# Optimization experiments

Hardware: AMD Instinct MI355X
Metric: run time of the kernel (lower is better)

## Reference

```python
import jax, jax.numpy as jnp
import numpy as np

D_MODEL = 512
N_HEADS = 8
D_HEAD = D_MODEL // N_HEADS  # 64
D_PROJ = 32
H_ENC = 512
D_MAX = 32


def _rope_cache(T, d):
    pos = jnp.arange(T, dtype=jnp.float32)[:, None]                      # [T,1]
    freqs = 1.0 / (10000.0 ** (jnp.arange(0, d, 2, dtype=jnp.float32) / d))  # [d/2]
    ang = pos * freqs                                                     # [T,d/2]
    return jnp.cos(ang), jnp.sin(ang)


def _apply_rope(x, cos, sin):
    # x: [B,H,T,D]
    T = x.shape[2]
    d2 = x.shape[-1] // 2
    x1, x2 = x[..., :d2], x[..., d2:]
    c = cos[:T][None, None]
    s = sin[:T][None, None]
    return jnp.concatenate([x1 * c - x2 * s, x2 * c + x1 * s], axis=-1)


def _layernorm(a, g, b, eps=1e-5):
    m = jnp.mean(a, axis=-1, keepdims=True)
    v = jnp.mean((a - m) ** 2, axis=-1, keepdims=True)
    return (a - m) * jax.lax.rsqrt(v + eps) * g + b


def setup_inputs() -> dict:
    key = jax.random.key(0)
    ks = jax.random.split(key, 8)
    B, T = 2, 2048
    x = jax.random.normal(ks[0], (B, T, D_MODEL), jnp.float32)
    q_projs = jax.random.normal(ks[1], (N_HEADS, D_MODEL, D_PROJ), jnp.float32) * D_MODEL ** -0.5
    k_projs = jax.random.normal(ks[2], (N_HEADS, D_MODEL, D_PROJ), jnp.float32) * D_MODEL ** -0.5
    w_v = jax.random.normal(ks[3], (D_MODEL, D_MODEL), jnp.float32) * D_MODEL ** -0.5
    w_proj = jax.random.normal(ks[4], (D_MODEL, D_MODEL), jnp.float32) * 0.02
    q_gain = jnp.ones((N_HEADS,), jnp.float32)
    enc_w0 = jax.random.normal(ks[5], (H_ENC, D_MODEL), jnp.float32) * D_MODEL ** -0.5
    enc_ln1_g = jnp.ones((H_ENC,), jnp.float32)
    enc_ln1_b = jnp.zeros((H_ENC,), jnp.float32)
    enc_w1 = jax.random.normal(ks[6], (H_ENC, H_ENC), jnp.float32) * H_ENC ** -0.5
    enc_ln2_g = jnp.ones((H_ENC,), jnp.float32)
    enc_ln2_b = jnp.zeros((H_ENC,), jnp.float32)
    enc_w2 = jax.random.normal(ks[7], (H_ENC, H_ENC), jnp.float32) * H_ENC ** -0.5
    enc_w_out = jax.random.normal(jax.random.fold_in(key, 99), (D_MAX, H_ENC), jnp.float32) * H_ENC ** -0.5
    coord_temp = jnp.ones((D_MAX,), jnp.float32)
    return {"x": x, "q_projs": q_projs, "k_projs": k_projs, "w_v": w_v, "w_proj": w_proj,
            "q_gain": q_gain, "enc_w0": enc_w0, "enc_ln1_g": enc_ln1_g, "enc_ln1_b": enc_ln1_b,
            "enc_w1": enc_w1, "enc_ln2_g": enc_ln2_g, "enc_ln2_b": enc_ln2_b, "enc_w2": enc_w2,
            "enc_w_out": enc_w_out, "coord_temp": coord_temp}


def reference(x, q_projs, k_projs, w_v, w_proj, q_gain,
              enc_w0, enc_ln1_g, enc_ln1_b, enc_w1, enc_ln2_g, enc_ln2_b,
              enc_w2, enc_w_out, coord_temp):
    B, T, C = x.shape
    # ---- CausalSelfAttention (qk_mode='per_head_proj') ----
    q = jnp.einsum('btd,hdo->bhto', x, q_projs)                    # [B,H,T,Dp]
    k = jnp.einsum('btd,hdo->bhto', x, k_projs)                    # [B,H,T,Dp]
    v = (x @ w_v.T).reshape(B, T, N_HEADS, D_HEAD).transpose(0, 2, 1, 3)  # [B,H,T,Dh]
    cos, sin = _rope_cache(T, D_PROJ)
    q = _apply_rope(q, cos, sin)
    k = _apply_rope(k, cos, sin)
    q = q * q_gain[None, :, None, None]
    scale = 1.0 / jnp.sqrt(jnp.asarray(D_PROJ, q.dtype))
    scores = jnp.einsum('bhto,bhso->bhts', q, k) * scale           # [B,H,T,T]
    causal = jnp.tril(jnp.ones((T, T), bool))
    scores = jnp.where(causal, scores, jnp.asarray(-1e30, scores.dtype))
    attn = jax.nn.softmax(scores, axis=-1)
    y = jnp.einsum('bhts,bhsd->bhtd', attn, v)                     # [B,H,T,Dh]
    # self-alignment subtraction (F.normalize eps = 1e-12)
    v_norm = v / jnp.maximum(jnp.linalg.norm(v, axis=-1, keepdims=True), 1e-12)
    self_align = jnp.sum(y * v_norm, axis=-1, keepdims=True) * v_norm
    y = y - self_align
    y = y.transpose(0, 2, 1, 3).reshape(B, T, C)
    h = x + y @ w_proj.T                                           # residual
    # ---- ChartEncoder (d_in == H so proj0 is Identity) ----
    he = h @ enc_w0.T
    he = h + jax.nn.silu(_layernorm(he, enc_ln1_g, enc_ln1_b) @ enc_w1.T)
    he = he + jax.nn.silu(_layernorm(he, enc_ln2_g, enc_ln2_b) @ enc_w2.T)
    h_rms = he * jax.lax.rsqrt(jnp.mean(he * he, axis=-1, keepdims=True) + 1e-6)
    z_raw = h_rms @ enc_w_out.T                                    # [B,T,d_max]
    z = jnp.tanh(z_raw / (jax.nn.softplus(coord_temp) + 1e-4))
    return z
```

## Files before the change

### kernel.cpp

```cpp
#include <hip/hip_runtime.h>
#include <math.h>

typedef unsigned short u16;
typedef __attribute__((ext_vector_type(8))) short short8;
typedef __attribute__((ext_vector_type(4))) float floatx4;

__device__ __forceinline__ float b2f(u16 u) { return __uint_as_float(((unsigned)u) << 16); }
__device__ __forceinline__ u16 f2b(float f) {
  unsigned u = __float_as_uint(f);
  return (u16)((u + 0x7fffu + ((u >> 16) & 1u)) >> 16);
}

__global__ __launch_bounds__(256) void prep_cast(const float* __restrict__ x, const float* __restrict__ wpr,
                                                 const float* __restrict__ w0, const float* __restrict__ w1,
                                                 const float* __restrict__ w2, const float* __restrict__ qp,
                                                 const float* __restrict__ kp, const float* __restrict__ wv,
                                                 u16* __restrict__ XB, u16* __restrict__ WPRb,
                                                 u16* __restrict__ W0b, u16* __restrict__ W1b,
                                                 u16* __restrict__ W2b, u16* __restrict__ wcat) {
  int bi = blockIdx.x, tid = threadIdx.x;
  if (bi < 2048) {
    int i = bi * 256 + tid;
    float4 v = ((const float4*)x)[i];
    ushort4 o; o.x = f2b(v.x); o.y = f2b(v.y); o.z = f2b(v.z); o.w = f2b(v.w);
    ((ushort4*)XB)[i] = o;
  } else if (bi < 3072) {
    int i = (bi - 2048) * 256 + tid;
    int sel = i >> 16, j = i & 65535;
    const float* s = sel == 0 ? wpr : sel == 1 ? w0 : sel == 2 ? w1 : w2;
    float4 v = ((const float4*)s)[j];
    ushort4 o; o.x = f2b(v.x); o.y = f2b(v.y); o.z = f2b(v.z); o.w = f2b(v.w);
    if (sel == 0) {
      ((ushort4*)WPRb)[j] = o;
    } else {
      u16* d = sel == 1 ? W0b : sel == 2 ? W1b : W2b;
      int n = j >> 7, k4 = (j & 127) << 2;
      int lane = (((k4 >> 3) & 3) << 4) | (n & 15);
      int dst = (((n >> 4) * 16 + (k4 >> 5)) << 9) + lane * 8 + (k4 & 7);
      *(ushort4*)(d + dst) = o;
    }
  } else {
    int i = (bi - 3072) * 256 + tid;
    int d = i & 511, c = i >> 9;
    float v;
    if (c < 512) {
      int hh = c >> 5, o = c & 31;
      const float* src = (hh < 8) ? qp : kp;
      int h = hh & 7;
      v = src[(h * 512 + d) * 32 + o];
    } else {
      v = wv[(c - 512) * 512 + d];
    }
    wcat[i] = f2b(v);
  }
}

template <int EPI, bool DUAL>
__global__ __launch_bounds__(256) void mgemm(const u16* __restrict__ A, const u16* __restrict__ Bw,
                                             const float* __restrict__ X, float* __restrict__ C,
                                             u16* __restrict__ Cb, int N) {
  __shared__ u16 As[64][72];
  __shared__ u16 Bs[64][72];
  const int tid = threadIdx.x;
  const int bm = blockIdx.y, bn = blockIdx.x;
  const int lane = tid & 63, wave = tid >> 6;
  const int wm = wave >> 1, wn = wave & 1;
  const int quad = lane >> 4, l16 = lane & 15;
  const int sr = tid >> 2;
  const int sk = (tid & 3) << 4;
  floatx4 acc[2][2] = {};
  const u16* Ap = A + (size_t)(bm * 64 + sr) * 512 + sk;
  const u16* Bp = Bw + (size_t)(bn * 64 + sr) * 512 + sk;
  uint4 a0 = *(const uint4*)(Ap);
  uint4 a1 = *(const uint4*)(Ap + 8);
  uint4 b0 = *(const uint4*)(Bp);
  uint4 b1 = *(const uint4*)(Bp + 8);
  for (int k0 = 0; k0 < 512; k0 += 64) {
    __syncthreads();
    *(uint4*)&As[sr][sk] = a0;
    *(uint4*)&As[sr][sk + 8] = a1;
    *(uint4*)&Bs[sr][sk] = b0;
    *(uint4*)&Bs[sr][sk + 8] = b1;
    __syncthreads();
    if (k0 + 64 < 512) {
      a0 = *(const uint4*)(Ap + k0 + 64);
      a1 = *(const uint4*)(Ap + k0 + 72);
      b0 = *(const uint4*)(Bp + k0 + 64);
      b1 = *(const uint4*)(Bp + k0 + 72);
    }
#pragma unroll
    for (int kk = 0; kk < 2; kk++) {
      short8 af0 = *(const short8*)&As[wm * 32 + l16][kk * 32 + quad * 8];
      short8 af1 = *(const short8*)&As[wm * 32 + 16 + l16][kk * 32 + quad * 8];
      short8 bf0 = *(const short8*)&Bs[wn * 32 + l16][kk * 32 + quad * 8];
      short8 bf1 = *(const short8*)&Bs[wn * 32 + 16 + l16][kk * 32 + quad * 8];
      acc[0][0] = __builtin_amdgcn_mfma_f32_16x16x32_bf16(af0, bf0, acc[0][0], 0, 0, 0);
      acc[0][1] = __builtin_amdgcn_mfma_f32_16x16x32_bf16(af0, bf1, acc[0][1], 0, 0, 0);
      acc[1][0] = __builtin_amdgcn_mfma_f32_16x16x32_bf16(af1, bf0, acc[1][0], 0, 0, 0);
      acc[1][1] = __builtin_amdgcn_mfma_f32_16x16x32_bf16(af1, bf1, acc[1][1], 0, 0, 0);
    }
  }
#pragma unroll
  for (int mt = 0; mt < 2; mt++)
#pragma unroll
    for (int r = 0; r < 4; r++) {
      int row = bm * 64 + wm * 32 + mt * 16 + quad * 4 + r;
#pragma unroll
      for (int nt = 0; nt < 2; nt++) {
        int col = bn * 64 + wn * 32 + nt * 16 + l16;
        float v = acc[mt][nt][r];
        if (EPI == 1) {
          v += X[(size_t)row * 512 + col];
        } else if (EPI == 2) {
          float xv = X[(size_t)row * 512 + col];
          v = xv + v / (1.f + __expf(-v));
        }
        C[(size_t)row * N + col] = v;
        if (DUAL) Cb[(size_t)row * N + col] = f2b(v);
      }
    }
}

__global__ __launch_bounds__(256) void prep_attn(const float* __restrict__ qkv, const float* __restrict__ qgain,
                                                 u16* __restrict__ qr, u16* __restrict__ kr,
                                                 u16* __restrict__ Vt) {
  const int bi = blockIdx.x, tid = threadIdx.x;
  if (bi < 2048) {
    int gid = bi * 256 + tid;
    int o = gid & 15;
    int t = (gid >> 4) & 2047;
    int h = (gid >> 15) & 7;
    int b = gid >> 18;
    const float* row = qkv + (size_t)(b * 2048 + t) * 1024;
    float freq = powf(10000.f, -(float)o / 16.f);
    float ang = (float)t * freq;
    float s, c;
    sincosf(ang, &s, &c);
    float g = qgain[h] * (0.17677669529663687f * 1.4426950408889634f);
    int qb = h * 32;
    float q0 = row[qb + o], q1 = row[qb + o + 16];
    float k0 = row[256 + qb + o], k1 = row[256 + qb + o + 16];
    u16* qo = qr + ((size_t)((b * 8 + h) * 2048 + t)) * 32;
    u16* ko = kr + ((size_t)((b * 8 + h) * 2048 + t)) * 32;
    qo[o] = f2b((q0 * c - q1 * s) * g);
    qo[o + 16] = f2b((q1 * c + q0 * s) * g);
    ko[o] = f2b(k0 * c - k1 * s);
    ko[o + 16] = f2b(k1 * c + k0 * s);
  } else {
    int idx = bi - 2048;
    const int tt = idx & 31, bh = idx >> 5;
    const int b = bh >> 3, h = bh & 7;
    __shared__ u16 Ts[64][72];
    const int r = tid >> 2, q = tid & 3;
    const float* src = qkv + ((size_t)(b * 2048 + tt * 64 + r)) * 1024 + 512 + h * 64 + q * 16;
#pragma unroll
    for (int j = 0; j < 4; j++) {
      float4 v = *(const float4*)(src + j * 4);
      Ts[q * 16 + j * 4 + 0][r] = f2b(v.x);
      Ts[q * 16 + j * 4 + 1][r] = f2b(v.y);
      Ts[q * 16 + j * 4 + 2][r] = f2b(v.z);
      Ts[q * 16 + j * 4 + 3][r] = f2b(v.w);
    }
    __syncthreads();
    u16* dst = Vt + ((size_t)(bh * 64 + r)) * 2048 + tt * 64 + q * 16;
    *(uint4*)dst = *(const uint4*)&Ts[r][q * 16];
    *(uint4*)(dst + 8) = *(const uint4*)&Ts[r][q * 16 + 8];
  }
}

__global__ __launch_bounds__(256) void attn_split(const u16* __restrict__ Qb, const u16* __restrict__ Kb,
                                                  const u16* __restrict__ Vt, float* __restrict__ PO,
                                                  float* __restrict__ PL) {
  const int bi = blockIdx.x;
  const int bh = bi & 15;
  const int q0i = (bi >> 4) & 15;
  const int rem = bi >> 8;
  const int qt = (rem & 1) ? (31 - q0i) : q0i;
  const int s = rem >> 1;
  const int tid = threadIdx.x;
  const int w = tid >> 6, lane = tid & 63, quad = lane >> 4, l16 = lane & 15;
  __shared__ u16 Vts[64][72];
  __shared__ u16 Ps[4][16][72];

  const int mid = (qt + 1) >> 1;
  const int kt_beg = s ? mid : 0;
  const int kt_end = s ? (qt + 1) : mid;

  short8 qfrag = *(const short8*)(Qb + ((size_t)(bh * 2048 + qt * 64 + w * 16 + l16)) * 32 + quad * 8);
  floatx4 o_acc[4] = {};
  float l_part[4] = {0.f, 0.f, 0.f, 0.f};
  const u16* Kbase = Kb + (size_t)bh * 2048 * 32;
  const u16* Vtb = Vt + (size_t)bh * 64 * 2048;
  const int vr = tid >> 2, vc = (tid & 3) << 4;

  uint4 v0 = {}, v1 = {};
  short8 kf[4] = {};
  if (kt_beg < kt_end) {
    const u16* src = Vtb + (size_t)vr * 2048 + kt_beg * 64 + vc;
    v0 = *(const uint4*)src;
    v1 = *(const uint4*)(src + 8);
#pragma unroll
    for (int nt = 0; nt < 4; nt++)
      kf[nt] = *(const short8*)(Kbase + (size_t)(kt_beg * 64 + nt * 16 + l16) * 32 + quad * 8);
  }

  for (int kt = kt_beg; kt < kt_end; ++kt) {
    __syncthreads();
    *(uint4*)&Vts[vr][vc] = v0;
    *(uint4*)&Vts[vr][vc + 8] = v1;
    __syncthreads();
    const bool more = (kt + 1 < kt_end);
    uint4 v0n = {}, v1n = {};
    short8 kfn[4] = {};
    if (more) {
      const u16* src = Vtb + (size_t)vr * 2048 + (kt + 1) * 64 + vc;
      v0n = *(const uint4*)src;
      v1n = *(const uint4*)(src + 8);
#pragma unroll
      for (int nt = 0; nt < 4; nt++)
        kfn[nt] = *(const short8*)(Kbase + (size_t)((kt + 1) * 64 + nt * 16 + l16) * 32 + quad * 8);
    }

    floatx4 s_acc[4];
#pragma unroll
    for (int nt = 0; nt < 4; nt++) {
      floatx4 zz = {0.f, 0.f, 0.f, 0.f};
      s_acc[nt] = __builtin_amdgcn_mfma_f32_16x16x32_bf16(qfrag, kf[nt], zz, 0, 0, 0);
    }
    const bool diag = (kt == qt);
#pragma unroll
    for (int r = 0; r < 4; r++) {
      int mloc = w * 16 + quad * 4 + r;
      float psum = 0.f;
#pragma unroll
      for (int nt = 0; nt < 4; nt++) {
        float p = __builtin_amdgcn_exp2f(s_acc[nt][r]);
        if (diag && (nt * 16 + l16) > mloc) p = 0.f;
        psum += p;
        Ps[w][quad * 4 + r][nt * 16 + l16] = f2b(p);
      }
      l_part[r] += psum;
    }
#pragma unroll
    for (int kc = 0; kc < 2; kc++) {
      short8 pf = *(const short8*)&Ps[w][l16][kc * 32 + quad * 8];
#pragma unroll
      for (int nt = 0; nt < 4; nt++) {
        short8 vf = *(const short8*)&Vts[nt * 16 + l16][kc * 32 + quad * 8];
        o_acc[nt] = __builtin_amdgcn_mfma_f32_16x16x32_bf16(pf, vf, o_acc[nt], 0, 0, 0);
      }
    }
    v0 = v0n; v1 = v1n;
#pragma unroll
    for (int nt = 0; nt < 4; nt++) kf[nt] = kfn[nt];
  }

  const int pidx = (bh * 32 + qt) * 2 + s;
  float* pob = PO + (size_t)pidx * 4096;
#pragma unroll
  for (int r = 0; r < 4; r++) {
    float ls = l_part[r];
#pragma unroll
    for (int mk = 1; mk < 16; mk <<= 1) ls += __shfl_xor(ls, mk, 64);
    int row = w * 16 + quad * 4 + r;
#pragma unroll
    for (int nt = 0; nt < 4; nt++) pob[row * 64 + nt * 16 + l16] = o_acc[nt][r];
    if (l16 == 0) PL[pidx * 64 + row] = ls;
  }
}

__global__ __launch_bounds__(256) void attn_combine(const float* __restrict__ PO, const float* __restrict__ PL,
                                                    const float* __restrict__ qkv, u16* __restrict__ y2b) {
  int ridx = blockIdx.x * 4 + (threadIdx.x >> 6);
  int lane = threadIdx.x & 63;
  int bh = ridx >> 11, tok = ridx & 2047;
  int qt = tok >> 6, row = tok & 63;
  int pidx = (bh * 32 + qt) * 2;
  const float* p0 = PO + (size_t)pidx * 4096 + row * 64;
  float o = p0[lane] + p0[4096 + lane];
  float l = PL[pidx * 64 + row] + PL[(pidx + 1) * 64 + row];
  float yv = o / l;
  int b = bh >> 3, h = bh & 7;
  float vv = qkv[(size_t)(b * 2048 + tok) * 1024 + 512 + h * 64 + lane];
  float ss = vv * vv, dot = yv * vv;
#pragma unroll
  for (int mk = 1; mk < 64; mk <<= 1) {
    ss += __shfl_xor(ss, mk, 64);
    dot += __shfl_xor(dot, mk, 64);
  }
  float coef = dot / fmaxf(ss, 1e-24f);
  y2b[(size_t)(b * 2048 + tok) * 512 + h * 64 + lane] = f2b(yv - coef * vv);
}

#define HPAD 516

__device__ __forceinline__ int enc_swz(int row, int col) {
  return row * 512 + ((((col >> 3) ^ (row & 7)) << 3) | (col & 7));
}

__device__ __forceinline__ void enc_gemm(const u16* __restrict__ inb, const u16* __restrict__ Wf,
                                         floatx4* acc, int wave, int l16, int quad, int lane) {
  const u16* wb = Wf + ((size_t)(wave * 4 * 16) << 9) + lane * 8;
  short8 aB[4];
  short8 bB[4][4];
#pragma unroll
  for (int p = 0; p < 4; p++) {
    aB[p] = *(const short8*)(inb + enc_swz(l16, p * 32 + quad * 8));
#pragma unroll
    for (int nt = 0; nt < 4; nt++)
      bB[p][nt] = *(const short8*)(wb + (((nt * 16) + p) << 9));
  }
#pragma unroll
  for (int ks = 0; ks < 16; ks++) {
    const int cur = ks & 3;
#pragma unroll
    for (int nt = 0; nt < 4; nt++)
      acc[nt] = __builtin_amdgcn_mfma_f32_16x16x32_bf16(aB[cur], bB[cur][nt], acc[nt], 0, 0, 0);
    if (ks + 4 < 16) {
      aB[cur] = *(const short8*)(inb + enc_swz(l16, (ks + 4) * 32 + quad * 8));
#pragma unroll
      for (int nt = 0; nt < 4; nt++)
        bB[cur][nt] = *(const short8*)(wb + (((nt * 16) + (ks + 4)) << 9));
    }
  }
}

__global__ __launch_bounds__(512) void enc_fused(const float* __restrict__ H, const u16* __restrict__ W0b,
                                                 const u16* __restrict__ W1b, const u16* __restrict__ W2b,
                                                 const float* __restrict__ g1v, const float* __restrict__ b1v,
                                                 const float* __restrict__ g2v, const float* __restrict__ b2v,
                                                 const float* __restrict__ wout, const float* __restrict__ ct,
                                                 float* __restrict__ z) {
  __shared__ u16 curb[16 * 512];
  __shared__ u16 lnb[16 * 512];
  __shared__ float hres[16][HPAD];
  __shared__ float red[8][16][2];

  const int tid = threadIdx.x;
  const int wave = tid >> 6, lane = tid & 63, quad = lane >> 4, l16 = lane & 15;
  const int row0 = blockIdx.x * 16;
  const int n0 = wave * 64;

#pragma unroll
  for (int j = 0; j < 4; j++) {
    int idx = j * 512 + tid;
    int row = idx >> 7, c4 = idx & 127;
    float4 v = ((const float4*)H)[(size_t)(row0 + row) * 128 + c4];
    *(float4*)&hres[row][c4 * 4] = v;
    int col = c4 * 4;
    curb[enc_swz(row, col + 0)] = f2b(v.x);
    curb[enc_swz(row, col + 1)] = f2b(v.y);
    curb[enc_swz(row, col + 2)] = f2b(v.z);
    curb[enc_swz(row, col + 3)] = f2b(v.w);
  }
  __syncthreads();

  floatx4 acc1[4] = {};
  enc_gemm(curb, W0b, acc1, wave, l16, quad, lane);

  {
#pragma unroll
    for (int r = 0; r < 4; r++) {
      float s = 0.f, q = 0.f;
#pragma unroll
      for (int nt = 0; nt < 4; nt++) { float v = acc1[nt][r]; s += v; q = fmaf(v, v, q); }
#pragma unroll
      for (int mk = 1; mk < 16; mk <<= 1) { s += __shfl_xor(s, mk, 64); q += __shfl_xor(q, mk, 64); }
      if (l16 == 0) { red[wave][quad * 4 + r][0] = s; red[wave][quad * 4 + r][1] = q; }
    }
    __syncthreads();
#pragma unroll
    for (int r = 0; r < 4; r++) {
      int R = quad * 4 + r;
      float st = 0.f, qt2 = 0.f;
#pragma unroll
      for (int w2 = 0; w2 < 8; w2++) { st += red[w2][R][0]; qt2 += red[w2][R][1]; }
      float mean = st * (1.f / 512.f);
      float inv = rsqrtf(qt2 * (1.f / 512.f) - mean * mean + 1e-5f);
#pragma unroll
      for (int nt = 0; nt < 4; nt++) {
        int col = n0 + nt * 16 + l16;
        lnb[enc_swz(R, col)] = f2b((acc1[nt][r] - mean) * inv * g1v[col] + b1v[col]);
      }
    }
    __syncthreads();
  }

  floatx4 acc2[4] = {};
  enc_gemm(lnb, W1b, acc2, wave, l16, quad, lane);
  float hval[4][4];
  {
#pragma unroll
    for (int r = 0; r < 4; r++) {
      int R = quad * 4 + r;
      float s = 0.f, q = 0.f;
#pragma unroll
      for (int nt = 0; nt < 4; nt++) {
        int col = n0 + nt * 16 + l16;
        float u = acc2[nt][r];
        float hv = hres[R][col] + u / (1.f + __expf(-u));
        hres[R][col] = hv;
        hval[nt][r] = hv;
        s += hv; q = fmaf(hv, hv, q);
      }
#pragma unroll
      for (int mk = 1; mk < 16; mk <<= 1) { s += __shfl_xor(s, mk, 64); q += __shfl_xor(q, mk, 64); }
      if (l16 == 0) { red[wave][R][0] = s; red[wave][R][1] = q; }
    }
    __syncthreads();
#pragma unroll
    for (int r = 0; r < 4; r++) {
      int R = quad * 4 + r;
      float st = 0.f, qt2 = 0.f;
#pragma unroll
      for (int w2 = 0; w2 < 8; w2++) { st += red[w2][R][0]; qt2 += red[w2][R][1]; }
      float mean = st * (1.f / 512.f);
      float inv = rsqrtf(qt2 * (1.f / 512.f) - mean * mean + 1e-5f);
#pragma unroll
      for (int nt = 0; nt < 4; nt++) {
        int col = n0 + nt * 16 + l16;
        lnb[enc_swz(R, col)] = f2b((hval[nt][r] - mean) * inv * g2v[col] + b2v[col]);
      }
    }
    __syncthreads();
  }

  floatx4 acc3[4] = {};
  enc_gemm(lnb, W2b, acc3, wave, l16, quad, lane);
  {
#pragma unroll
    for (int r = 0; r < 4; r++) {
      int R = quad * 4 + r;
      float q = 0.f;
#pragma unroll
      for (int nt = 0; nt < 4; nt++) {
        int col = n0 + nt * 16 + l16;
        float u = acc3[nt][r];
        float hv = hres[R][col] + u / (1.f + __expf(-u));
        hres[R][col] = hv;
        q = fmaf(hv, hv, q);
      }
#pragma unroll
      for (int mk = 1; mk < 16; mk <<= 1) q += __shfl_xor(q, mk, 64);
      if (l16 == 0) red[wave][R][1] = q;
    }
    __syncthreads();
  }

  {
    const int n = lane & 31, kh = lane >> 5;
    float rinv[2], pacc[2] = {0.f, 0.f};
#pragma unroll
    for (int rr = 0; rr < 2; rr++) {
      int R = wave * 2 + rr;
      float qt2 = 0.f;
#pragma unroll
      for (int w2 = 0; w2 < 8; w2++) qt2 += red[w2][R][1];
      rinv[rr] = rsqrtf(qt2 * (1.f / 512.f) + 1e-6f);
    }
    for (int kc = 0; kc < 64; kc++) {
      int k = kh * 256 + kc * 4;
      float4 wv = *(const float4*)(wout + (size_t)n * 512 + k);
#pragma unroll
      for (int rr = 0; rr < 2; rr++) {
        float4 hv = *(const float4*)&hres[wave * 2 + rr][k];
        pacc[rr] = fmaf(wv.x, hv.x, fmaf(wv.y, hv.y, fmaf(wv.z, hv.z, fmaf(wv.w, hv.w, pacc[rr]))));
      }
    }
#pragma unroll
    for (int rr = 0; rr < 2; rr++) pacc[rr] += __shfl_xor(pacc[rr], 32, 64);
    if (kh == 0) {
      float c = ct[n];
      float sp = (c > 20.f) ? c : log1pf(__expf(c));
#pragma unroll
      for (int rr = 0; rr < 2; rr++)
        z[(size_t)(row0 + wave * 2 + rr) * 32 + n] = tanhf(pacc[rr] * rinv[rr] / (sp + 1e-4f));
    }
  }
}

extern "C" void kernel_launch(void* const* d_in, const int* in_sizes, int n_in,
                              void* d_out, int out_size, void* d_ws, size_t ws_size,
                              hipStream_t stream) {
  const float* x = (const float*)d_in[0];
  const float* qp = (const float*)d_in[1];
  const float* kp = (const float*)d_in[2];
  const float* wv = (const float*)d_in[3];
  const float* wpr = (const float*)d_in[4];
  const float* qg = (const float*)d_in[5];
  const float* w0 = (const float*)d_in[6];
  const float* g1 = (const float*)d_in[7];
  const float* b1 = (const float*)d_in[8];
  const float* w1 = (const float*)d_in[9];
  const float* g2 = (const float*)d_in[10];
  const float* b2 = (const float*)d_in[11];
  const float* w2 = (const float*)d_in[12];
  const float* wout = (const float*)d_in[13];
  const float* ct = (const float*)d_in[14];
  float* z = (float*)d_out;

  float* ws = (float*)d_ws;
  const size_t MEG = 1024 * 1024;
  float* A_QKV = ws;
  u16* A_Qb = (u16*)(ws + 4 * MEG);
  u16* A_Kb = (u16*)(ws + 4 * MEG + 524288);
  u16* A_Vt = (u16*)(ws + 5 * MEG);
  float* A_PO = ws + 6 * MEG;
  u16* A_Y2b = (u16*)(ws + 10 * MEG);
  float* A_H = ws + 11 * MEG;
  u16* XB = (u16*)(ws + 13 * MEG);
  float* A_PL = ws + 13 * MEG;
  u16* WCATb = (u16*)(ws + 14 * MEG);
  u16* WPRb = WCATb + 524288;
  u16* W0b = WPRb + 262144;
  u16* W1b = W0b + 262144;
  u16* W2b = W1b + 262144;

  hipLaunchKernelGGL(prep_cast, dim3(5120), dim3(256), 0, stream, x, wpr, w0, w1, w2, qp, kp, wv,
                     XB, WPRb, W0b, W1b, W2b, WCATb);
  hipLaunchKernelGGL((mgemm<0, false>), dim3(16, 64), dim3(256), 0, stream, XB, WCATb,
                     (const float*)nullptr, A_QKV, (u16*)nullptr, 1024);
  hipLaunchKernelGGL(prep_attn, dim3(2560), dim3(256), 0, stream, A_QKV, qg, A_Qb, A_Kb, A_Vt);
  hipLaunchKernelGGL(attn_split, dim3(1024), dim3(256), 0, stream, A_Qb, A_Kb, A_Vt, A_PO, A_PL);
  hipLaunchKernelGGL(attn_combine, dim3(8192), dim3(256), 0, stream, A_PO, A_PL, A_QKV, A_Y2b);
  hipLaunchKernelGGL((mgemm<1, false>), dim3(8, 64), dim3(256), 0, stream, A_Y2b, WPRb, x, A_H,
                     (u16*)nullptr, 512);
  hipLaunchKernelGGL(enc_fused, dim3(256), dim3(512), 0, stream, A_H, W0b, W1b, W2b,
                     g1, b1, g2, b2, wout, ct, z);
}
```

Measured before the change: 191.7 us.

## Stream encoder weights through LDS with double-buffered direct global-to-LDS loads

Replaces per-wave register prefetch of the weight fragments (a 4-deep software pipeline in registers) with asynchronous global_load_lds copies into a double-buffered LDS staging area, one k-chunk ahead. The aim is to cut register pressure and overlap weight fetch with MFMA work. In exchange it adds 64 KB of shared memory per block, which lowers occupancy, and a block-wide barrier on every k step. Prefetch depth also drops from four chunks to one.

```diff
diff --git a/kernel.cpp b/kernel.cpp
--- a/kernel.cpp
+++ b/kernel.cpp
@@ -299,29 +299,34 @@
 }
 
 __device__ __forceinline__ void enc_gemm(const u16* __restrict__ inb, const u16* __restrict__ Wf,
-                                         floatx4* acc, int wave, int l16, int quad, int lane) {
-  const u16* wb = Wf + ((size_t)(wave * 4 * 16) << 9) + lane * 8;
-  short8 aB[4];
-  short8 bB[4][4];
-#pragma unroll
-  for (int p = 0; p < 4; p++) {
-    aB[p] = *(const short8*)(inb + enc_swz(l16, p * 32 + quad * 8));
-#pragma unroll
-    for (int nt = 0; nt < 4; nt++)
-      bB[p][nt] = *(const short8*)(wb + (((nt * 16) + p) << 9));
-  }
-#pragma unroll
-  for (int ks = 0; ks < 16; ks++) {
-    const int cur = ks & 3;
-#pragma unroll
-    for (int nt = 0; nt < 4; nt++)
-      acc[nt] = __builtin_amdgcn_mfma_f32_16x16x32_bf16(aB[cur], bB[cur][nt], acc[nt], 0, 0, 0);
-    if (ks + 4 < 16) {
-      aB[cur] = *(const short8*)(inb + enc_swz(l16, (ks + 4) * 32 + quad * 8));
+                                         u16* __restrict__ Wst, floatx4* acc,
+                                         int wave, int lane, int l16, int quad) {
+  const int wslot = (wave * 4) * 512;
+  const int src_lane = lane * 8;
+#pragma unroll
+  for (int nt = 0; nt < 4; nt++)
+    __builtin_amdgcn_global_load_lds(
+        (const __attribute__((address_space(1))) void*)(Wf + ((size_t)((wave * 4 + nt) * 16) << 9) + src_lane),
+        (__attribute__((address_space(3))) void*)(Wst + wslot + nt * 512), 16, 0, 0);
+  __syncthreads();
+  for (int kc = 0; kc < 16; kc++) {
+    const int cb = kc & 1;
+    u16* bufC = Wst + cb * (8 * 4 * 512) + wslot;
+    if (kc + 1 < 16) {
+      u16* bufN = Wst + (cb ^ 1) * (8 * 4 * 512) + wslot;
 #pragma unroll
       for (int nt = 0; nt < 4; nt++)
-        bB[cur][nt] = *(const short8*)(wb + (((nt * 16) + (ks + 4)) << 9));
-    }
+        __builtin_amdgcn_global_load_lds(
+            (const __attribute__((address_space(1))) void*)(Wf + ((size_t)((wave * 4 + nt) * 16 + kc + 1) << 9) + src_lane),
+            (__attribute__((address_space(3))) void*)(bufN + nt * 512), 16, 0, 0);
+    }
+    short8 af = *(const short8*)(inb + enc_swz(l16, kc * 32 + quad * 8));
+#pragma unroll
+    for (int nt = 0; nt < 4; nt++) {
+      short8 bf = *(const short8*)(bufC + nt * 512 + src_lane);
+      acc[nt] = __builtin_amdgcn_mfma_f32_16x16x32_bf16(af, bf, acc[nt], 0, 0, 0);
+    }
+    __syncthreads();
   }
 }
 
@@ -333,6 +338,7 @@
                                                  float* __restrict__ z) {
   __shared__ u16 curb[16 * 512];
   __shared__ u16 lnb[16 * 512];
+  __shared__ u16 Wst[2 * 8 * 4 * 512];
   __shared__ float hres[16][HPAD];
   __shared__ float red[8][16][2];
 
@@ -356,7 +362,7 @@
   __syncthreads();
 
   floatx4 acc1[4] = {};
-  enc_gemm(curb, W0b, acc1, wave, l16, quad, lane);
+  enc_gemm(curb, W0b, Wst, acc1, wave, lane, l16, quad);
 
   {
 #pragma unroll
@@ -387,7 +393,7 @@
   }
 
   floatx4 acc2[4] = {};
-  enc_gemm(lnb, W1b, acc2, wave, l16, quad, lane);
+  enc_gemm(lnb, W1b, Wst, acc2, wave, lane, l16, quad);
   float hval[4][4];
   {
 #pragma unroll
@@ -426,7 +432,7 @@
   }
 
   floatx4 acc3[4] = {};
-  enc_gemm(lnb, W2b, acc3, wave, l16, quad, lane);
+  enc_gemm(lnb, W2b, Wst, acc3, wave, lane, l16, quad);
   {
 #pragma unroll
     for (int r = 0; r < 4; r++) {
```

Result: slower. 202.1 us (+5.4%).
